# Optimization experiments

Hardware: AMD Instinct MI355X
Metric: run time of the kernel (lower is better)

The kernel has to match this reference:

```python
import jax, jax.numpy as jnp
import numpy as np

B, S, SV = 4, 2048, 50
QF = KF = VF = E = 1024
SCALE = np.float32(np.power(KF, 0.5))


def setup_inputs() -> dict:
    key = jax.random.key(0)
    ks = jax.random.split(key, 8)
    s = 0.02
    return {
        "Q": jax.random.normal(ks[0], (B, S, QF), dtype=jnp.float32),
        "K": jax.random.normal(ks[1], (B, S, KF), dtype=jnp.float32),
        "V": jax.random.normal(ks[2], (B, SV, VF), dtype=jnp.float32),
        # weights stored [in, out] so forward is x @ W (== torch Linear with weight.T)
        "W_Q": jax.random.normal(ks[3], (QF, E), dtype=jnp.float32) * s,
        "W_K": jax.random.normal(ks[4], (KF, E), dtype=jnp.float32) * s,
        "W_v": jax.random.normal(ks[5], (E, E), dtype=jnp.float32) * s,
        "W_vq": jax.random.normal(ks[6], (SV, E), dtype=jnp.float32) * s,
        "W_vk": jax.random.normal(ks[7], (SV, E), dtype=jnp.float32) * s,
    }


def reference(Q, K, V, W_Q, W_K, W_v, W_vq, W_vk):
    # mode == 'mode2', dropout=None (inference path)
    q = jnp.tanh(Q) @ W_Q          # [B,S,E]
    k = jnp.tanh(K) @ W_K          # [B,S,E]
    v = jnp.tanh(V) @ W_v          # [B,SV,E]

    qk = jnp.einsum('bse,bte->bst', q, k) / SCALE   # [B,S,S]
    vq = jnp.einsum('bse,bve->bsv', q, v) / SCALE   # [B,S,SV]
    vk = jnp.einsum('bse,bve->bsv', k, v) / SCALE   # [B,S,SV]

    f = jax.nn.softmax(qk, axis=-1)                 # [B,S,S]
    g = 1.0 - f

    q2 = jnp.einsum('bst,bte->bse', f, q) + vq @ W_vq
    k2 = jnp.einsum('bst,bte->bse', g, k) + vk @ W_vk

    Q_out = jnp.einsum('bst,bte->bse', f, q2)
    K_out = jnp.einsum('bst,bte->bse', g, k2)
    return (Q_out, K_out, f)
```

## Files before the change

### kernel.cpp

```cpp
#include <hip/hip_runtime.h>
#include <cstdint>
#include <cstddef>

typedef __bf16 bf16_t;
typedef __bf16 bf16x4 __attribute__((ext_vector_type(4)));
typedef __bf16 bf16x8 __attribute__((ext_vector_type(8)));
typedef float floatx4 __attribute__((ext_vector_type(4)));

#define B_ 4
#define S_ 2048
#define E_ 1024
#define SV_ 50
#define SVP_ 64
#define BSE_ ((long)B_ * S_ * E_)

__device__ __forceinline__ void async_copy16(const bf16_t* g, bf16_t* l) {
  __builtin_amdgcn_global_load_lds(
      (const __attribute__((address_space(1))) void*)g,
      (__attribute__((address_space(3))) void*)l, 16, 0, 0);
}

__global__ __launch_bounds__(256) void tanh2_k(const float* __restrict__ Q,
                                               const float* __restrict__ Kin,
                                               bf16_t* __restrict__ out) {
  long i4 = ((long)blockIdx.x * 256 + threadIdx.x) * 4;
  const long n = (long)B_ * S_ * E_;
  const float* src = (i4 < n) ? (Q + i4) : (Kin + (i4 - n));
  float4 x = *(const float4*)src;
  bf16x4 o;
  o[0] = (bf16_t)tanhf(x.x);
  o[1] = (bf16_t)tanhf(x.y);
  o[2] = (bf16_t)tanhf(x.z);
  o[3] = (bf16_t)tanhf(x.w);
  *(bf16x4*)&out[i4] = o;
}

__global__ __launch_bounds__(256) void tanh_vpad_k(const float* __restrict__ V,
                                                   bf16_t* __restrict__ out) {
  int i = blockIdx.x * 256 + threadIdx.x;
  int e = i & 1023, r = (i >> 10) & 63, b = i >> 16;
  float v = 0.f;
  if (r < SV_) v = tanhf(V[((long)(b * SV_ + r) << 10) + e]);
  out[i] = (bf16_t)v;
}

__global__ __launch_bounds__(256) void transp_cast3_k(const float* __restrict__ W0,
                                                      const float* __restrict__ W1,
                                                      const float* __restrict__ W2,
                                                      bf16_t* __restrict__ out,
                                                      int K, int N, int Kp) {
  __shared__ float tile[32][33];
  const float* W = (blockIdx.z == 0) ? W0 : (blockIdx.z == 1) ? W1 : W2;
  bf16_t* o = out + (long)blockIdx.z * N * Kp;
  int k0 = blockIdx.y * 32, n0 = blockIdx.x * 32;
  int tx = threadIdx.x, ty = threadIdx.y;
#pragma unroll
  for (int s2 = 0; s2 < 4; ++s2) {
    int kk = ty + s2 * 8;
    float v = 0.f;
    if (k0 + kk < K && n0 + tx < N) v = W[(long)(k0 + kk) * N + n0 + tx];
    tile[kk][tx] = v;
  }
  __syncthreads();
#pragma unroll
  for (int s2 = 0; s2 < 4; ++s2) {
    int nn = ty + s2 * 8;
    if (n0 + nn < N && k0 + tx < Kp)
      o[(long)(n0 + nn) * Kp + k0 + tx] = (bf16_t)tile[tx][nn];
  }
}

__global__ __launch_bounds__(256) void transp2_bf16_k(const bf16_t* __restrict__ in,
                                                      long selIn, long inRow,
                                                      long inBatch,
                                                      bf16_t* __restrict__ out,
                                                      long selOut, long outRow,
                                                      long outBatch) {
  __shared__ bf16_t tile[32][33];
  int r0 = blockIdx.y * 32, c0 = blockIdx.x * 32;
  int tx = threadIdx.x, ty = threadIdx.y;
  int half = blockIdx.z & 1, bz = blockIdx.z >> 1;
  long ib = (long)bz * inBatch + (long)half * selIn;
  long ob = (long)bz * outBatch + (long)half * selOut;
#pragma unroll
  for (int s2 = 0; s2 < 4; ++s2)
    tile[ty + s2 * 8][tx] = in[ib + (long)(r0 + ty + s2 * 8) * inRow + c0 + tx];
  __syncthreads();
#pragma unroll
  for (int s2 = 0; s2 < 4; ++s2)
    out[ob + (long)(c0 + ty + s2 * 8) * outRow + r0 + tx] = tile[tx][ty + s2 * 8];
}

__global__ __launch_bounds__(256) void colsum_part_k(const bf16_t* __restrict__ X,
                                                     long rowStride, long batchStride,
                                                     float* __restrict__ part) {
  int e = blockIdx.x * 256 + threadIdx.x;
  int chunk = blockIdx.y, b = blockIdx.z;
  const bf16_t* p = X + (long)b * batchStride + (long)chunk * 256 * rowStride + e;
  float s = 0.f;
#pragma unroll 8
  for (int t = 0; t < 256; ++t) s += (float)p[(long)t * rowStride];
  part[((long)b * 8 + chunk) * E_ + e] = s;
}

__global__ __launch_bounds__(256) void colsum_fin_k(const float* __restrict__ part,
                                                    float* __restrict__ out) {
  int e = blockIdx.x * 256 + threadIdx.x;
  int b = blockIdx.y;
  float s = 0.f;
#pragma unroll
  for (int c = 0; c < 8; ++c) s += part[((long)b * 8 + c) * E_ + e];
  out[(long)b * E_ + e] = s;
}

__global__ __launch_bounds__(256) void softmax_row_k(bf16_t* __restrict__ fb,
                                                     float* __restrict__ Fout) {
  long off = ((long)blockIdx.y * S_ + blockIdx.x) * S_;
  int t = threadIdx.x;
  bf16x8 xb = *(const bf16x8*)&fb[off + 8 * t];
  float x[8];
#pragma unroll
  for (int i = 0; i < 8; ++i) x[i] = (float)xb[i];
  float mx = fmaxf(fmaxf(fmaxf(x[0], x[1]), fmaxf(x[2], x[3])),
                   fmaxf(fmaxf(x[4], x[5]), fmaxf(x[6], x[7])));
#pragma unroll
  for (int s = 32; s >= 1; s >>= 1) mx = fmaxf(mx, __shfl_xor(mx, s));
  __shared__ float red[4];
  int wv = t >> 6;
  if ((t & 63) == 0) red[wv] = mx;
  __syncthreads();
  mx = fmaxf(fmaxf(red[0], red[1]), fmaxf(red[2], red[3]));
  float e[8];
  float sum = 0.f;
#pragma unroll
  for (int i = 0; i < 8; ++i) {
    e[i] = __expf(x[i] - mx);
    sum += e[i];
  }
#pragma unroll
  for (int s = 32; s >= 1; s >>= 1) sum += __shfl_xor(sum, s);
  __shared__ float red2[4];
  if ((t & 63) == 0) red2[wv] = sum;
  __syncthreads();
  float inv = 1.0f / ((red2[0] + red2[1]) + (red2[2] + red2[3]));
  bf16x8 ob;
#pragma unroll
  for (int i = 0; i < 8; ++i) {
    e[i] *= inv;
    ob[i] = (bf16_t)e[i];
  }
  *(float4*)&Fout[off + 8 * t] = make_float4(e[0], e[1], e[2], e[3]);
  *(float4*)&Fout[off + 8 * t + 4] = make_float4(e[4], e[5], e[6], e[7]);
  *(bf16x8*)&fb[off + 8 * t] = ob;
}

__global__ __launch_bounds__(256) void gemm_vqk_k(const bf16_t* __restrict__ qkb,
                                                  const bf16_t* __restrict__ vb,
                                                  bf16_t* __restrict__ vqkf) {
  __shared__ __align__(16) bf16_t As[64 * 64];
  __shared__ __align__(16) bf16_t Bs[64 * 64];
  const int zz = blockIdx.z;
  const int sel = zz >> 2;
  const int b = zz & 3;
  const bf16_t* Ab = qkb + (long)sel * BSE_ + (long)b * S_ * E_;
  const bf16_t* Bb = vb + (long)b * SVP_ * E_;
  bf16_t* outB = vqkf + ((long)b * 2 + sel) * ((long)S_ * SVP_);
  const int t = threadIdx.x;
  const int lane = t & 63;
  const int wave = t >> 6;
  const int wm = (wave & 1) * 32;
  const int wn = (wave >> 1) * 32;
  const long rowBase = (long)blockIdx.y * 64;

  floatx4 acc[2][2];
#pragma unroll
  for (int i = 0; i < 2; ++i)
#pragma unroll
    for (int j = 0; j < 2; ++j) acc[i][j] = {0.f, 0.f, 0.f, 0.f};

  const int sr = t >> 3;
  const int sc = (t & 7) * 8;
  for (int k0 = 0; k0 < E_; k0 += 64) {
#pragma unroll
    for (int p = 0; p < 2; ++p) {
      int r = p * 32 + sr;
      *(uint4*)&As[r * 64 + sc] = *(const uint4*)&Ab[(rowBase + r) * E_ + k0 + sc];
      *(uint4*)&Bs[r * 64 + sc] = *(const uint4*)&Bb[(long)r * E_ + k0 + sc];
    }
    __syncthreads();
#pragma unroll
    for (int ks = 0; ks < 64; ks += 32) {
      const int fr = lane & 15;
      const int fk = ks + ((lane >> 4) << 3);
      bf16x8 a0 = *(const bf16x8*)&As[(wm + fr) * 64 + fk];
      bf16x8 a1 = *(const bf16x8*)&As[(wm + 16 + fr) * 64 + fk];
      bf16x8 b0 = *(const bf16x8*)&Bs[(wn + fr) * 64 + fk];
      bf16x8 b1 = *(const bf16x8*)&Bs[(wn + 16 + fr) * 64 + fk];
      acc[0][0] = __builtin_amdgcn_mfma_f32_16x16x32_bf16(a0, b0, acc[0][0], 0, 0, 0);
      acc[0][1] = __builtin_amdgcn_mfma_f32_16x16x32_bf16(a0, b1, acc[0][1], 0, 0, 0);
      acc[1][0] = __builtin_amdgcn_mfma_f32_16x16x32_bf16(a1, b0, acc[1][0], 0, 0, 0);
      acc[1][1] = __builtin_amdgcn_mfma_f32_16x16x32_bf16(a1, b1, acc[1][1], 0, 0, 0);
    }
    __syncthreads();
  }

  const int cr = lane & 15;
  const int rq = (lane >> 4) * 4;
  const float alpha = sel ? -1.f / 32.f : 1.f / 32.f;
#pragma unroll
  for (int i = 0; i < 2; ++i)
#pragma unroll
    for (int j = 0; j < 2; ++j)
#pragma unroll
      for (int r = 0; r < 4; ++r) {
        long row = rowBase + wm + i * 16 + rq + r;
        int col = wn + j * 16 + cr;
        outB[row * SVP_ + col] = (bf16_t)(alpha * acc[i][j][r]);
      }
}

__global__ __launch_bounds__(256) void gemm_fused_k(
    const bf16_t* __restrict__ A1, long sA1,
    const bf16_t* __restrict__ B1, long sB1,
    int N, int K1,
    const bf16_t* __restrict__ A2q, const bf16_t* __restrict__ A2k, long sA2,
    const bf16_t* __restrict__ B2,
    float alpha, int negSplit, const float* __restrict__ colVec, long sV,
    float* __restrict__ outFa, bf16_t* __restrict__ outBa, int lda, long sOa,
    float* __restrict__ outFb, bf16_t* __restrict__ outBb, int ldb, long sOb,
    int capZ, int capM) {
  __shared__ __align__(16) bf16_t As[2 * 128 * 64];
  __shared__ __align__(16) bf16_t Bs[2 * 128 * 64];
  const int t = threadIdx.x;
  const int lane = t & 63;
  const int wave = t >> 6;
  const int wm = (wave & 1) * 64;
  const int wn = (wave >> 1) * 64;
  const long b = blockIdx.z;
  const long rowBase = (long)blockIdx.y * 128;
  const long colBase = (long)blockIdx.x * 128;
  if ((int)b >= capZ && rowBase >= capM) return;
  const bf16_t* Ab = A1 + b * sA1;
  const bf16_t* Bb = B1 + b * sB1;

  floatx4 acc[4][4];
#pragma unroll
  for (int i = 0; i < 4; ++i)
#pragma unroll
    for (int j = 0; j < 4; ++j) acc[i][j] = {0.f, 0.f, 0.f, 0.f};

  const int srow = lane >> 3;
  const int schunk = (lane & 7) ^ srow;
  const bf16_t* aG[4];
  const bf16_t* bG[4];
  int lofs[4];
#pragma unroll
  for (int i = 0; i < 4; ++i) {
    int r = wave * 32 + i * 8;
    aG[i] = Ab + (rowBase + r + srow) * (long)K1 + schunk * 8;
    bG[i] = Bb + (colBase + r + srow) * (long)K1 + schunk * 8;
    lofs[i] = r * 64;
  }

  const int fr = lane & 15;
  const int hi = lane >> 4;
  int aoff[4], boff[4];
#pragma unroll
  for (int i = 0; i < 4; ++i) {
    aoff[i] = (wm + i * 16 + fr) * 64 + ((hi ^ (fr & 7)) * 8);
    boff[i] = (wn + i * 16 + fr) * 64 + ((hi ^ (fr & 7)) * 8);
  }

  const int nK1 = K1 >> 6;
  const int nt = nK1 + (A2q ? 1 : 0);

  auto stage = [&](int buf, int kt) {
    const int bo = buf * (128 * 64);
    if (kt < nK1) {
      const long k0 = (long)kt * 64;
#pragma unroll
      for (int i = 0; i < 4; ++i) {
        async_copy16(aG[i] + k0, &As[bo + lofs[i]]);
        async_copy16(bG[i] + k0, &Bs[bo + lofs[i]]);
      }
    } else {
      const bf16_t* A2 = (colBase >= negSplit) ? A2k : A2q;
      const bf16_t* A2b = A2 + b * sA2;
#pragma unroll
      for (int i = 0; i < 4; ++i) {
        int r = wave * 32 + i * 8;
        async_copy16(A2b + (rowBase + r + srow) * 64 + schunk * 8, &As[bo + lofs[i]]);
        async_copy16(B2 + (colBase + r + srow) * 64 + schunk * 8, &Bs[bo + lofs[i]]);
      }
    }
  };

  stage(0, 0);
  if (nt > 1) stage(1, 1);

  for (int kt = 0; kt < nt; ++kt) {
    if (kt < nt - 1)
      asm volatile("s_waitcnt vmcnt(8)" ::: "memory");
    else
      asm volatile("s_waitcnt vmcnt(0)" ::: "memory");
    __builtin_amdgcn_s_barrier();
    __builtin_amdgcn_sched_barrier(0);
    const int bo = (kt & 1) * (128 * 64);
    __builtin_amdgcn_s_setprio(1);
#pragma unroll
    for (int ks = 0; ks < 64; ks += 32) {
      bf16x8 af[4], bfr[4];
#pragma unroll
      for (int i = 0; i < 4; ++i) af[i] = *(const bf16x8*)&As[bo + (aoff[i] ^ ks)];
#pragma unroll
      for (int i = 0; i < 4; ++i) bfr[i] = *(const bf16x8*)&Bs[bo + (boff[i] ^ ks)];
#pragma unroll
      for (int i = 0; i < 4; ++i)
#pragma unroll
        for (int j = 0; j < 4; ++j)
          acc[i][j] =
              __builtin_amdgcn_mfma_f32_16x16x32_bf16(af[i], bfr[j], acc[i][j], 0, 0, 0);
    }
    __builtin_amdgcn_s_setprio(0);
    __builtin_amdgcn_sched_barrier(0);
    __builtin_amdgcn_s_barrier();
    __builtin_amdgcn_sched_barrier(0);
    if (kt + 2 < nt) stage(kt & 1, kt + 2);
  }

  const int cr = lane & 15;
  const int rq = hi * 4;
  const bool neg = (colBase >= negSplit);
  const float* cv = colVec ? (colVec + b * sV + (neg ? colBase - negSplit : colBase))
                           : nullptr;
  float* oF = neg ? outFb : outFa;
  bf16_t* oB = neg ? outBb : outBa;
  const int ld = neg ? ldb : lda;
  const long sO = neg ? sOb : sOa;
  const long cb0 = neg ? (long)(colBase - negSplit) : colBase;
#pragma unroll
  for (int i = 0; i < 4; ++i)
#pragma unroll
    for (int j = 0; j < 4; ++j)
#pragma unroll
      for (int r = 0; r < 4; ++r) {
        long row = rowBase + wm + i * 16 + rq + r;
        int c = wn + j * 16 + cr;
        float v = alpha * acc[i][j][r];
        if (neg) v = cv[c] - v;
        long o = b * sO + row * (long)ld + cb0 + c;
        if (oF) oF[o] = v;
        if (oB) oB[o] = (bf16_t)v;
      }
}

extern "C" void kernel_launch(void* const* d_in, const int* in_sizes, int n_in,
                              void* d_out, int out_size, void* d_ws, size_t ws_size,
                              hipStream_t stream) {
  const float* Q = (const float*)d_in[0];
  const float* Kin = (const float*)d_in[1];
  const float* V = (const float*)d_in[2];
  const float* W_Q = (const float*)d_in[3];
  const float* W_K = (const float*)d_in[4];
  const float* W_v = (const float*)d_in[5];
  const float* W_vq = (const float*)d_in[6];
  const float* W_vk = (const float*)d_in[7];

  float* Qout = (float*)d_out;
  float* Kout = Qout + (long)B_ * S_ * E_;
  float* Fout = Kout + (long)B_ * S_ * E_;

  char* w = (char*)d_ws;
  auto alloc = [&](size_t bytes) {
    char* p = w;
    w += (bytes + 255) & ~(size_t)255;
    return p;
  };
  const long BSE = BSE_;
  bf16_t* WQKt = (bf16_t*)alloc((size_t)2 * 2 * E_ * E_);
  bf16_t* WVt = (bf16_t*)alloc((size_t)2 * E_ * E_);
  bf16_t* Wv2T = (bf16_t*)alloc((size_t)2 * 2 * E_ * SVP_);
  bf16_t* QtKt = (bf16_t*)alloc((size_t)2 * 2 * BSE);
  bf16_t* Vt = (bf16_t*)alloc((size_t)2 * B_ * SVP_ * E_);
  bf16_t* qkb = (bf16_t*)alloc((size_t)2 * 2 * BSE);
  bf16_t* vb = (bf16_t*)alloc((size_t)2 * B_ * SVP_ * E_);
  bf16_t* qkT = (bf16_t*)alloc((size_t)2 * (long)B_ * 2 * E_ * S_);
  bf16_t* fb = (bf16_t*)alloc((size_t)2 * (long)B_ * S_ * S_);
  bf16_t* vqkf = (bf16_t*)alloc((size_t)2 * (long)B_ * 2 * S_ * SVP_);
  bf16_t* q2k2 = (bf16_t*)alloc((size_t)2 * (long)B_ * S_ * 2 * E_);
  bf16_t* q2k2T = (bf16_t*)alloc((size_t)2 * (long)B_ * 2 * E_ * S_);
  float* part = (float*)alloc((size_t)4 * B_ * 8 * E_);
  float* ck = (float*)alloc((size_t)4 * B_ * E_);
  float* ck2 = (float*)alloc((size_t)4 * B_ * E_);

  bf16_t* qb = qkb;
  bf16_t* kb = qkb + BSE;

  dim3 blk256(256);
  dim3 blk32x8(32, 8);

  transp_cast3_k<<<dim3(32, 32, 3), blk32x8, 0, stream>>>(W_Q, W_K, W_v, WQKt,
                                                          E_, E_, E_);
  transp_cast3_k<<<dim3(32, 2, 2), blk32x8, 0, stream>>>(W_vq, W_vk, W_vq, Wv2T,
                                                         SV_, E_, SVP_);

  tanh2_k<<<dim3((unsigned)(2 * BSE / 1024)), blk256, 0, stream>>>(Q, Kin, QtKt);
  tanh_vpad_k<<<dim3(B_ * SVP_ * E_ / 256), blk256, 0, stream>>>(V, Vt);

  gemm_fused_k<<<dim3(E_ / 128, B_ * S_ / 128, 3), blk256, 0, stream>>>(
      QtKt, BSE, WQKt, (long)E_ * E_, E_, E_,
      nullptr, nullptr, 0, nullptr, 1.f, E_, nullptr, 0,
      nullptr, qkb, E_, BSE, nullptr, nullptr, 0, 0,
      2, B_ * SVP_);

  transp2_bf16_k<<<dim3(E_ / 32, S_ / 32, 2 * B_), blk32x8, 0, stream>>>(
      qkb, BSE, E_, (long)S_ * E_, qkT, (long)E_ * S_, S_, (long)2 * E_ * S_);

  gemm_fused_k<<<dim3(S_ / 128, S_ / 128, B_), blk256, 0, stream>>>(
      qb, (long)S_ * E_, kb, (long)S_ * E_, S_, E_,
      nullptr, nullptr, 0, nullptr, 1.f / 32.f, S_, nullptr, 0,
      nullptr, fb, S_, (long)S_ * S_, nullptr, nullptr, 0, 0,
      9999, 0);
  softmax_row_k<<<dim3(S_, B_), blk256, 0, stream>>>(fb, Fout);

  colsum_part_k<<<dim3(E_ / 256, 8, B_), blk256, 0, stream>>>(kb, E_, (long)S_ * E_, part);
  colsum_fin_k<<<dim3(E_ / 256, B_), blk256, 0, stream>>>(part, ck);

  gemm_vqk_k<<<dim3(1, S_ / 64, 2 * B_), blk256, 0, stream>>>(qkb, vb, vqkf);

  gemm_fused_k<<<dim3(2 * E_ / 128, S_ / 128, B_), blk256, 0, stream>>>(
      fb, (long)S_ * S_, qkT, (long)2 * E_ * S_, 2 * E_, S_,
      vqkf, vqkf + (long)S_ * SVP_, (long)2 * S_ * SVP_, Wv2T,
      1.f, E_, ck, E_,
      nullptr, q2k2, 2 * E_, (long)S_ * 2 * E_,
      nullptr, q2k2 + E_, 2 * E_, (long)S_ * 2 * E_,
      9999, 0);

  transp2_bf16_k<<<dim3(E_ / 32, S_ / 32, 2 * B_), blk32x8, 0, stream>>>(
      q2k2, E_, 2 * E_, (long)S_ * 2 * E_, q2k2T, (long)E_ * S_, S_,
      (long)2 * E_ * S_);

  colsum_part_k<<<dim3(E_ / 256, 8, B_), blk256, 0, stream>>>(
      q2k2 + E_, 2 * E_, (long)S_ * 2 * E_, part);
  colsum_fin_k<<<dim3(E_ / 256, B_), blk256, 0, stream>>>(part, ck2);

  gemm_fused_k<<<dim3(2 * E_ / 128, S_ / 128, B_), blk256, 0, stream>>>(
      fb, (long)S_ * S_, q2k2T, (long)2 * E_ * S_, 2 * E_, S_,
      nullptr, nullptr, 0, nullptr,
      1.f, E_, ck2, E_,
      Qout, nullptr, E_, (long)S_ * E_,
      Kout, nullptr, E_, (long)S_ * E_,
      9999, 0);
}
```

Measured before the change: 604.3 us.

## Fuse column sums into transposes and shrink GEMM K-tile to 32

Column sums of k and k2, previously computed by separate two-pass kernels, are now produced inside the transpose kernel using shared-memory partials and atomicAdd into zeroed buffers. This removes four launches and an extra read of the matrices. Separately, the GEMM K-tile is halved from 64 to 32 with a simpler unswizzled LDS layout and launch_bounds(256,4), aiming for higher occupancy at the cost of more barriers per K, possible LDS bank conflicts, and non-deterministic float atomics.

```diff
diff --git a/kernel.cpp b/kernel.cpp
--- a/kernel.cpp
+++ b/kernel.cpp
@@ -75,42 +75,33 @@
                                                       long inBatch,
                                                       bf16_t* __restrict__ out,
                                                       long selOut, long outRow,
-                                                      long outBatch) {
+                                                      long outBatch,
+                                                      float* __restrict__ csum) {
   __shared__ bf16_t tile[32][33];
+  __shared__ float cs[8][32];
   int r0 = blockIdx.y * 32, c0 = blockIdx.x * 32;
   int tx = threadIdx.x, ty = threadIdx.y;
   int half = blockIdx.z & 1, bz = blockIdx.z >> 1;
   long ib = (long)bz * inBatch + (long)half * selIn;
   long ob = (long)bz * outBatch + (long)half * selOut;
-#pragma unroll
-  for (int s2 = 0; s2 < 4; ++s2)
-    tile[ty + s2 * 8][tx] = in[ib + (long)(r0 + ty + s2 * 8) * inRow + c0 + tx];
+  float ps = 0.f;
+#pragma unroll
+  for (int s2 = 0; s2 < 4; ++s2) {
+    bf16_t v = in[ib + (long)(r0 + ty + s2 * 8) * inRow + c0 + tx];
+    tile[ty + s2 * 8][tx] = v;
+    ps += (float)v;
+  }
+  cs[ty][tx] = ps;
   __syncthreads();
 #pragma unroll
   for (int s2 = 0; s2 < 4; ++s2)
     out[ob + (long)(c0 + ty + s2 * 8) * outRow + r0 + tx] = tile[tx][ty + s2 * 8];
-}
-
-__global__ __launch_bounds__(256) void colsum_part_k(const bf16_t* __restrict__ X,
-                                                     long rowStride, long batchStride,
-                                                     float* __restrict__ part) {
-  int e = blockIdx.x * 256 + threadIdx.x;
-  int chunk = blockIdx.y, b = blockIdx.z;
-  const bf16_t* p = X + (long)b * batchStride + (long)chunk * 256 * rowStride + e;
-  float s = 0.f;
-#pragma unroll 8
-  for (int t = 0; t < 256; ++t) s += (float)p[(long)t * rowStride];
-  part[((long)b * 8 + chunk) * E_ + e] = s;
-}
-
-__global__ __launch_bounds__(256) void colsum_fin_k(const float* __restrict__ part,
-                                                    float* __restrict__ out) {
-  int e = blockIdx.x * 256 + threadIdx.x;
-  int b = blockIdx.y;
-  float s = 0.f;
-#pragma unroll
-  for (int c = 0; c < 8; ++c) s += part[((long)b * 8 + c) * E_ + e];
-  out[(long)b * E_ + e] = s;
+  if (csum && half == 1 && ty == 0) {
+    float s = 0.f;
+#pragma unroll
+    for (int c = 0; c < 8; ++c) s += cs[c][tx];
+    atomicAdd(&csum[(long)bz * E_ + c0 + tx], s);
+  }
 }
 
 __global__ __launch_bounds__(256) void softmax_row_k(bf16_t* __restrict__ fb,
@@ -219,7 +210,7 @@
       }
 }
 
-__global__ __launch_bounds__(256) void gemm_fused_k(
+__global__ __launch_bounds__(256, 4) void gemm_fused_k(
     const bf16_t* __restrict__ A1, long sA1,
     const bf16_t* __restrict__ B1, long sB1,
     int N, int K1,
@@ -229,8 +220,8 @@
     float* __restrict__ outFa, bf16_t* __restrict__ outBa, int lda, long sOa,
     float* __restrict__ outFb, bf16_t* __restrict__ outBb, int ldb, long sOb,
     int capZ, int capM) {
-  __shared__ __align__(16) bf16_t As[2 * 128 * 64];
-  __shared__ __align__(16) bf16_t Bs[2 * 128 * 64];
+  __shared__ __align__(16) bf16_t As[2 * 128 * 32];
+  __shared__ __align__(16) bf16_t Bs[2 * 128 * 32];
   const int t = threadIdx.x;
   const int lane = t & 63;
   const int wave = t >> 6;
@@ -249,48 +240,44 @@
 #pragma unroll
     for (int j = 0; j < 4; ++j) acc[i][j] = {0.f, 0.f, 0.f, 0.f};
 
-  const int srow = lane >> 3;
-  const int schunk = (lane & 7) ^ srow;
-  const bf16_t* aG[4];
-  const bf16_t* bG[4];
-  int lofs[4];
-#pragma unroll
-  for (int i = 0; i < 4; ++i) {
-    int r = wave * 32 + i * 8;
-    aG[i] = Ab + (rowBase + r + srow) * (long)K1 + schunk * 8;
-    bG[i] = Bb + (colBase + r + srow) * (long)K1 + schunk * 8;
-    lofs[i] = r * 64;
-  }
+  const int srow = lane >> 2;
+  const int sch = lane & 3;
+  const bf16_t* aG = Ab + (rowBase + wave * 16 + srow) * (long)K1 + sch * 8;
+  const bf16_t* bG = Bb + (colBase + wave * 16 + srow) * (long)K1 + sch * 8;
+  const long rStepA = (long)64 * K1;
+  const int ldsW = (wave * 16) * 32;
 
   const int fr = lane & 15;
   const int hi = lane >> 4;
   int aoff[4], boff[4];
 #pragma unroll
   for (int i = 0; i < 4; ++i) {
-    aoff[i] = (wm + i * 16 + fr) * 64 + ((hi ^ (fr & 7)) * 8);
-    boff[i] = (wn + i * 16 + fr) * 64 + ((hi ^ (fr & 7)) * 8);
-  }
-
-  const int nK1 = K1 >> 6;
-  const int nt = nK1 + (A2q ? 1 : 0);
+    aoff[i] = (wm + i * 16 + fr) * 32 + hi * 8;
+    boff[i] = (wn + i * 16 + fr) * 32 + hi * 8;
+  }
+
+  const int nK1 = K1 >> 5;
+  const int nt = nK1 + (A2q ? 2 : 0);
 
   auto stage = [&](int buf, int kt) {
-    const int bo = buf * (128 * 64);
+    const int bo = buf * (128 * 32);
     if (kt < nK1) {
-      const long k0 = (long)kt * 64;
-#pragma unroll
-      for (int i = 0; i < 4; ++i) {
-        async_copy16(aG[i] + k0, &As[bo + lofs[i]]);
-        async_copy16(bG[i] + k0, &Bs[bo + lofs[i]]);
+      const long k0 = (long)kt * 32;
+#pragma unroll
+      for (int p = 0; p < 2; ++p) {
+        async_copy16(aG + p * rStepA + k0, &As[bo + p * 64 * 32 + ldsW]);
+        async_copy16(bG + p * rStepA + k0, &Bs[bo + p * 64 * 32 + ldsW]);
       }
     } else {
+      const int ts = kt - nK1;
       const bf16_t* A2 = (colBase >= negSplit) ? A2k : A2q;
       const bf16_t* A2b = A2 + b * sA2;
 #pragma unroll
-      for (int i = 0; i < 4; ++i) {
-        int r = wave * 32 + i * 8;
-        async_copy16(A2b + (rowBase + r + srow) * 64 + schunk * 8, &As[bo + lofs[i]]);
-        async_copy16(B2 + (colBase + r + srow) * 64 + schunk * 8, &Bs[bo + lofs[i]]);
+      for (int p = 0; p < 2; ++p) {
+        long r = rowBase + p * 64 + wave * 16 + srow;
+        long rc = colBase + p * 64 + wave * 16 + srow;
+        async_copy16(A2b + r * 64 + ts * 32 + sch * 8, &As[bo + p * 64 * 32 + ldsW]);
+        async_copy16(B2 + rc * 64 + ts * 32 + sch * 8, &Bs[bo + p * 64 * 32 + ldsW]);
       }
     }
   };
@@ -300,20 +287,19 @@
 
   for (int kt = 0; kt < nt; ++kt) {
     if (kt < nt - 1)
-      asm volatile("s_waitcnt vmcnt(8)" ::: "memory");
+      asm volatile("s_waitcnt vmcnt(4)" ::: "memory");
     else
       asm volatile("s_waitcnt vmcnt(0)" ::: "memory");
     __builtin_amdgcn_s_barrier();
     __builtin_amdgcn_sched_barrier(0);
-    const int bo = (kt & 1) * (128 * 64);
+    const int bo = (kt & 1) * (128 * 32);
     __builtin_amdgcn_s_setprio(1);
-#pragma unroll
-    for (int ks = 0; ks < 64; ks += 32) {
+    {
       bf16x8 af[4], bfr[4];
 #pragma unroll
-      for (int i = 0; i < 4; ++i) af[i] = *(const bf16x8*)&As[bo + (aoff[i] ^ ks)];
-#pragma unroll
-      for (int i = 0; i < 4; ++i) bfr[i] = *(const bf16x8*)&Bs[bo + (boff[i] ^ ks)];
+      for (int i = 0; i < 4; ++i) af[i] = *(const bf16x8*)&As[bo + aoff[i]];
+#pragma unroll
+      for (int i = 0; i < 4; ++i) bfr[i] = *(const bf16x8*)&Bs[bo + boff[i]];
 #pragma unroll
       for (int i = 0; i < 4; ++i)
 #pragma unroll
@@ -389,7 +375,6 @@
   bf16_t* vqkf = (bf16_t*)alloc((size_t)2 * (long)B_ * 2 * S_ * SVP_);
   bf16_t* q2k2 = (bf16_t*)alloc((size_t)2 * (long)B_ * S_ * 2 * E_);
   bf16_t* q2k2T = (bf16_t*)alloc((size_t)2 * (long)B_ * 2 * E_ * S_);
-  float* part = (float*)alloc((size_t)4 * B_ * 8 * E_);
   float* ck = (float*)alloc((size_t)4 * B_ * E_);
   float* ck2 = (float*)alloc((size_t)4 * B_ * E_);
 
@@ -398,6 +383,8 @@
 
   dim3 blk256(256);
   dim3 blk32x8(32, 8);
+
+  hipMemsetAsync(ck, 0, (size_t)2 * 4 * B_ * E_, stream);
 
   transp_cast3_k<<<dim3(32, 32, 3), blk32x8, 0, stream>>>(W_Q, W_K, W_v, WQKt,
                                                           E_, E_, E_);
@@ -414,7 +401,7 @@
       2, B_ * SVP_);
 
   transp2_bf16_k<<<dim3(E_ / 32, S_ / 32, 2 * B_), blk32x8, 0, stream>>>(
-      qkb, BSE, E_, (long)S_ * E_, qkT, (long)E_ * S_, S_, (long)2 * E_ * S_);
+      qkb, BSE, E_, (long)S_ * E_, qkT, (long)E_ * S_, S_, (long)2 * E_ * S_, ck);
 
   gemm_fused_k<<<dim3(S_ / 128, S_ / 128, B_), blk256, 0, stream>>>(
       qb, (long)S_ * E_, kb, (long)S_ * E_, S_, E_,
@@ -422,9 +409,6 @@
       nullptr, fb, S_, (long)S_ * S_, nullptr, nullptr, 0, 0,
       9999, 0);
   softmax_row_k<<<dim3(S_, B_), blk256, 0, stream>>>(fb, Fout);
-
-  colsum_part_k<<<dim3(E_ / 256, 8, B_), blk256, 0, stream>>>(kb, E_, (long)S_ * E_, part);
-  colsum_fin_k<<<dim3(E_ / 256, B_), blk256, 0, stream>>>(part, ck);
 
   gemm_vqk_k<<<dim3(1, S_ / 64, 2 * B_), blk256, 0, stream>>>(qkb, vb, vqkf);
 
@@ -438,11 +422,7 @@
 
   transp2_bf16_k<<<dim3(E_ / 32, S_ / 32, 2 * B_), blk32x8, 0, stream>>>(
       q2k2, E_, 2 * E_, (long)S_ * 2 * E_, q2k2T, (long)E_ * S_, S_,
-      (long)2 * E_ * S_);
-
-  colsum_part_k<<<dim3(E_ / 256, 8, B_), blk256, 0, stream>>>(
-      q2k2 + E_, 2 * E_, (long)S_ * 2 * E_, part);
-  colsum_fin_k<<<dim3(E_ / 256, B_), blk256, 0, stream>>>(part, ck2);
+      (long)2 * E_ * S_, ck2);
 
   gemm_fused_k<<<dim3(2 * E_ / 128, S_ / 128, B_), blk256, 0, stream>>>(
       fb, (long)S_ * S_, q2k2T, (long)2 * E_ * S_, 2 * E_, S_,
```

After: 579.6 us. 4.1% less time.
